# Optimization experiments

Hardware: AMD Instinct MI355X
Metric: run time of the kernel (lower is better)

## Reference

```python
import jax, jax.numpy as jnp
import numpy as np

D_MODEL = 1024
HEADS = 16
DILATION = 4
LN_EPS = 1e-5


def setup_inputs() -> dict:
    key = jax.random.key(0)
    ks = jax.random.split(key, 11)
    B, S, D = 2, 4096, D_MODEL
    x = jax.random.normal(ks[0], (B, S, D), dtype=jnp.float32)
    def lin(k):
        kw, kb = jax.random.split(k)
        W = jax.random.normal(kw, (D, D), dtype=jnp.float32) * 0.02  # torch Linear layout [out, in]
        b = jax.random.normal(kb, (D,), dtype=jnp.float32) * 0.02
        return W, b
    Wq, bq = lin(ks[1])
    Wk, bk = lin(ks[2])
    Wv, bv = lin(ks[3])
    Wf, bf = lin(ks[4])
    gamma = jnp.ones((D,), dtype=jnp.float32)
    beta = jnp.zeros((D,), dtype=jnp.float32)
    return {"x": x, "Wq": Wq, "bq": bq, "Wk": Wk, "bk": bk,
            "Wv": Wv, "bv": bv, "Wf": Wf, "bf": bf,
            "gamma": gamma, "beta": beta}


def _layer_norm(x, gamma, beta):
    mu = jnp.mean(x, axis=-1, keepdims=True)
    var = jnp.mean(jnp.square(x - mu), axis=-1, keepdims=True)
    return (x - mu) * jax.lax.rsqrt(var + LN_EPS) * gamma + beta


def reference(x, Wq, bq, Wk, bk, Wv, bv, Wf, bf, gamma, beta):
    B, S, D = x.shape
    dil, H = DILATION, HEADS
    dh = D // H
    pad = (-S) % dil  # padding_size
    xp = jnp.pad(x, ((0, 0), (0, pad), (0, 0)))
    Sp = S + pad
    L = Sp // dil
    # strided (atrous) regrouping: [B, Sp, D] -> [B*dil, L, D]
    xr = xp.reshape(B, L, dil, D).transpose(0, 2, 1, 3).reshape(B * dil, L, D)
    q = xr @ Wq.T + bq
    k = xr @ Wk.T + bk
    v = xr @ Wv.T + bv
    # split heads: [B*dil, H, L, dh]
    q = q.reshape(B * dil, L, H, dh).transpose(0, 2, 1, 3)
    k = k.reshape(B * dil, L, H, dh).transpose(0, 2, 1, 3)
    v = v.reshape(B * dil, L, H, dh).transpose(0, 2, 1, 3)
    scores = jnp.einsum('bhqd,bhkd->bhqk', q, k) / jnp.sqrt(jnp.float32(dh))
    probs = jax.nn.softmax(scores, axis=-1)
    ctx = jnp.einsum('bhqk,bhkd->bhqd', probs, v)
    # merge heads and undo atrous regrouping
    ctx = ctx.transpose(0, 2, 1, 3).reshape(B * dil, L, D)
    ctx = ctx.reshape(B, dil, L, D).transpose(0, 2, 1, 3).reshape(B, Sp, D)
    ctx = ctx[:, :S]
    atted = ctx @ Wf.T + bf  # dropout p=0.0
    final = _layer_norm(atted + x, gamma, beta)
    return (final, atted)
```

## Files before the change

### kernel.cpp

```cpp
#include <hip/hip_runtime.h>
#include <hip/hip_bf16.h>
#include <cstdint>
#include <cstddef>

constexpr int B_  = 2;
constexpr int S_  = 4096;
constexpr int D_  = 1024;
constexpr int H_  = 16;
constexpr int DH_ = 64;
constexpr int DIL = 4;
constexpr int L_  = S_ / DIL;
constexpr int M_  = B_ * S_;

typedef __attribute__((ext_vector_type(8))) short short8;
typedef __attribute__((ext_vector_type(4))) float f32x4;

__device__ __forceinline__ unsigned short f2b(float f) {
    union { float f; unsigned u; } v;
    v.f = f;
    unsigned r = v.u + 0x7fff + ((v.u >> 16) & 1);
    return (unsigned short)(r >> 16);
}

__device__ __forceinline__ unsigned pkbf(float a, float b) {
    float2 t; t.x = a; t.y = b;
    __hip_bfloat162 h = __float22bfloat162_rn(t);
    union { __hip_bfloat162 h; unsigned u; } c; c.h = h;
    return c.u;
}

__device__ __forceinline__ int xcd_swz(int orig, int nwg) {
    int q = nwg >> 3, r = nwg & 7;
    int xcd = orig & 7, idx = orig >> 3;
    return (xcd < r ? xcd * (q + 1) : r * (q + 1) + (xcd - r) * q) + idx;
}

#define GLOAD16(gptr, lptr)                                                    \
    __builtin_amdgcn_global_load_lds(                                          \
        (const __attribute__((address_space(1))) void*)(gptr),                 \
        (__attribute__((address_space(3))) void*)(lptr), 16, 0, 0)

__global__ __launch_bounds__(256)
void conv_f2b(const float* __restrict__ in, unsigned short* __restrict__ out, int n4) {
    int i = blockIdx.x * 256 + threadIdx.x;
    if (i < n4) {
        float4 v = reinterpret_cast<const float4*>(in)[i];
        ushort4 o;
        o.x = f2b(v.x); o.y = f2b(v.y); o.z = f2b(v.z); o.w = f2b(v.w);
        reinterpret_cast<ushort4*>(out)[i] = o;
    }
}

__global__ __launch_bounds__(256)
void conv_w4(const float* __restrict__ w0, const float* __restrict__ w1,
             const float* __restrict__ w2, const float* __restrict__ w3,
             unsigned short* __restrict__ out) {
    int bid = blockIdx.x;
    int which = bid >> 10;
    const float* src = (which == 0) ? w0 : (which == 1) ? w1 : (which == 2) ? w2 : w3;
    int i = (bid & 1023) * 256 + threadIdx.x;
    float4 v = reinterpret_cast<const float4*>(src)[i];
    ushort4 o;
    o.x = f2b(v.x); o.y = f2b(v.y); o.z = f2b(v.z); o.w = f2b(v.w);
    reinterpret_cast<ushort4*>(out + (size_t)which * D_ * D_)[i] = o;
}

template <int OUT_BF16>
__global__ __launch_bounds__(256)
void gemm_mfma(const unsigned short* __restrict__ A,
               const unsigned short* __restrict__ W,
               const float* __restrict__ bias,
               void* __restrict__ Cout, int M, int N, int K) {
    __shared__ unsigned short As[2][128 * 64];
    __shared__ unsigned short Bs[2][128 * 64];

    const int tid  = threadIdx.x;
    const int lane = tid & 63, wave = tid >> 6;
    const int l15 = lane & 15, l4 = lane >> 4;
    const int wr = wave >> 1, wc = wave & 1;
    const int gx = N >> 7;
    const int wg = xcd_swz(blockIdx.x, gridDim.x);
    const int bm = (wg / gx) * 128, bn = (wg % gx) * 128;

    auto stage = [&](int k0, int buf) {
        #pragma unroll
        for (int i = 0; i < 4; ++i) {
            int ch = i * 256 + wave * 64 + lane;
            int r = ch >> 3, c8 = ch & 7;
            const unsigned short* ga = A + (size_t)(bm + r) * K + k0 + c8 * 8;
            GLOAD16(ga, (char*)&As[buf][0] + (size_t)(i * 256 + wave * 64) * 16);
            const unsigned short* gb = W + (size_t)(bn + r) * K + k0 + c8 * 8;
            GLOAD16(gb, (char*)&Bs[buf][0] + (size_t)(i * 256 + wave * 64) * 16);
        }
    };

    f32x4 acc[4][4] = {};

    stage(0, 0);
    __syncthreads();
    int cur = 0;

    for (int k0 = 0; k0 < K; k0 += 64) {
        if (k0 + 64 < K) stage(k0 + 64, cur ^ 1);

        #pragma unroll
        for (int ks = 0; ks < 2; ++ks) {
            short8 af[4], bf[4];
            #pragma unroll
            for (int mi = 0; mi < 4; ++mi)
                af[mi] = *reinterpret_cast<const short8*>(
                    &As[cur][(wr * 64 + mi * 16 + l15) * 64 + ks * 32 + l4 * 8]);
            #pragma unroll
            for (int ni = 0; ni < 4; ++ni)
                bf[ni] = *reinterpret_cast<const short8*>(
                    &Bs[cur][(wc * 64 + ni * 16 + l15) * 64 + ks * 32 + l4 * 8]);
            #pragma unroll
            for (int mi = 0; mi < 4; ++mi)
                #pragma unroll
                for (int ni = 0; ni < 4; ++ni)
                    acc[mi][ni] = __builtin_amdgcn_mfma_f32_16x16x32_bf16(
                        af[mi], bf[ni], acc[mi][ni], 0, 0, 0);
        }
        __syncthreads();
        cur ^= 1;
    }

    #pragma unroll
    for (int ni = 0; ni < 4; ++ni) {
        int col = bn + wc * 64 + ni * 16 + l15;
        float bv = bias[col];
        #pragma unroll
        for (int mi = 0; mi < 4; ++mi) {
            #pragma unroll
            for (int r = 0; r < 4; ++r) {
                int row = bm + wr * 64 + mi * 16 + l4 * 4 + r;
                float v = acc[mi][ni][r] + bv;
                if (OUT_BF16)
                    ((unsigned short*)Cout)[(size_t)row * N + col] = f2b(v);
                else
                    ((float*)Cout)[(size_t)row * N + col] = v;
            }
        }
    }
}

__global__ __launch_bounds__(256)
void gemm_qkv(const unsigned short* __restrict__ A,
              const unsigned short* __restrict__ W,
              const float* __restrict__ bq, const float* __restrict__ bk,
              const float* __restrict__ bv,
              unsigned short* __restrict__ Qb, unsigned short* __restrict__ Kb,
              unsigned short* __restrict__ Vb, int M, int K) {
    __shared__ unsigned short As[2][128 * 64];
    __shared__ unsigned short Bs[2][128 * 64];

    const int tid  = threadIdx.x;
    const int lane = tid & 63, wave = tid >> 6;
    const int l15 = lane & 15, l4 = lane >> 4;
    const int wr = wave >> 1, wc = wave & 1;
    const int gx = 24;
    const int wg = xcd_swz(blockIdx.x, gridDim.x);
    const int bm = (wg / gx) * 128, bn = (wg % gx) * 128;

    auto stage = [&](int k0, int buf) {
        #pragma unroll
        for (int i = 0; i < 4; ++i) {
            int ch = i * 256 + wave * 64 + lane;
            int r = ch >> 3, c8 = ch & 7;
            const unsigned short* ga = A + (size_t)(bm + r) * K + k0 + c8 * 8;
            GLOAD16(ga, (char*)&As[buf][0] + (size_t)(i * 256 + wave * 64) * 16);
            const unsigned short* gb = W + (size_t)(bn + r) * K + k0 + c8 * 8;
            GLOAD16(gb, (char*)&Bs[buf][0] + (size_t)(i * 256 + wave * 64) * 16);
        }
    };

    f32x4 acc[4][4] = {};

    stage(0, 0);
    __syncthreads();
    int cur = 0;

    for (int k0 = 0; k0 < K; k0 += 64) {
        if (k0 + 64 < K) stage(k0 + 64, cur ^ 1);

        #pragma unroll
        for (int ks = 0; ks < 2; ++ks) {
            short8 af[4], bf[4];
            #pragma unroll
            for (int mi = 0; mi < 4; ++mi)
                af[mi] = *reinterpret_cast<const short8*>(
                    &As[cur][(wr * 64 + mi * 16 + l15) * 64 + ks * 32 + l4 * 8]);
            #pragma unroll
            for (int ni = 0; ni < 4; ++ni)
                bf[ni] = *reinterpret_cast<const short8*>(
                    &Bs[cur][(wc * 64 + ni * 16 + l15) * 64 + ks * 32 + l4 * 8]);
            #pragma unroll
            for (int mi = 0; mi < 4; ++mi)
                #pragma unroll
                for (int ni = 0; ni < 4; ++ni)
                    acc[mi][ni] = __builtin_amdgcn_mfma_f32_16x16x32_bf16(
                        af[mi], bf[ni], acc[mi][ni], 0, 0, 0);
        }
        __syncthreads();
        cur ^= 1;
    }

    const int seg = bn >> 10;
    const float* bp = (seg == 0) ? bq : (seg == 1) ? bk : bv;
    unsigned short* ob = (seg == 0) ? Qb : (seg == 1) ? Kb : Vb;
    const float qs = (seg == 0) ? 0.125f : 1.0f;
    const int cb = bn & 1023;

    #pragma unroll
    for (int ni = 0; ni < 4; ++ni) {
        int col = cb + wc * 64 + ni * 16 + l15;
        float bvv = bp[col];
        #pragma unroll
        for (int mi = 0; mi < 4; ++mi) {
            #pragma unroll
            for (int r = 0; r < 4; ++r) {
                int row = bm + wr * 64 + mi * 16 + l4 * 4 + r;
                ob[(size_t)row * 1024 + col] = f2b((acc[mi][ni][r] + bvv) * qs);
            }
        }
    }
}

__global__ __launch_bounds__(256)
void tvt(const unsigned short* __restrict__ Vb, unsigned short* __restrict__ Vtg) {
    __shared__ unsigned short Ts[64 * 64];
    const int tid = threadIdx.x;
    const int blk = blockIdx.x;
    const int lt = blk & 15;
    const int h  = (blk >> 4) & 15;
    const int bd = blk >> 8;
    const int b = bd >> 2, dd = bd & 3;
    const size_t rowbase = (size_t)b * S_;

    #pragma unroll
    for (int i = 0; i < 2; ++i) {
        int ch = i * 256 + tid;
        int lloc = ch >> 3, c8 = ch & 7;
        short8 v = *reinterpret_cast<const short8*>(
            Vb + (rowbase + (size_t)(lt * 64 + lloc) * DIL + dd) * D_ + h * 64 + c8 * 8);
        #pragma unroll
        for (int j = 0; j < 8; ++j) {
            int dh = c8 * 8 + j;
            Ts[dh * 64 + (((lloc >> 3) ^ (dh & 7)) * 8) + (lloc & 7)] = (unsigned short)v[j];
        }
    }
    __syncthreads();

    const size_t obase = ((size_t)(bd * 16 + h) * 64) * L_;
    #pragma unroll
    for (int i = 0; i < 2; ++i) {
        int ch = i * 256 + tid;
        int dh = ch >> 3, c = ch & 7;
        uint4 val = *reinterpret_cast<const uint4*>(&Ts[dh * 64 + ((c ^ (dh & 7)) * 8)]);
        *reinterpret_cast<uint4*>(Vtg + obase + (size_t)dh * L_ + lt * 64 + c * 8) = val;
    }
}

__global__ __launch_bounds__(256)
void attn_mfma(const unsigned short* __restrict__ Q,
               const unsigned short* __restrict__ K,
               const unsigned short* __restrict__ Vtg,
               unsigned short* __restrict__ O) {
    __shared__ unsigned short Ks[2][64 * 64];
    __shared__ unsigned short Vs[2][64 * 64];
    __shared__ unsigned short Ps[4][1024];

    const int tid = threadIdx.x;
    const int lane = tid & 63, wave = tid >> 6;
    const int l15 = lane & 15, l4 = lane >> 4;
    const int blk = xcd_swz(blockIdx.x, gridDim.x);
    const int qt = blk & 15;
    const int h  = (blk >> 4) & 15;
    const int bd = blk >> 8;
    const int b = bd >> 2, dd = bd & 3;
    const size_t rowbase = (size_t)b * S_;
    const int colbase = h * DH_;

    short8 qf[2];
    {
        int q = qt * 64 + wave * 16 + l15;
        const unsigned short* qp =
            Q + (rowbase + (size_t)q * DIL + dd) * D_ + colbase;
        qf[0] = *reinterpret_cast<const short8*>(qp + l4 * 8);
        qf[1] = *reinterpret_cast<const short8*>(qp + 32 + l4 * 8);
    }

    const unsigned short* vbase = Vtg + ((size_t)(bd * 16 + h) * 64) * L_;

    auto stageK = [&](int kt, int buf) {
        #pragma unroll
        for (int i = 0; i < 2; ++i) {
            int key = i * 32 + wave * 8 + (lane >> 3);
            int srcc = (lane & 7) ^ (lane >> 3);
            const unsigned short* g =
                K + (rowbase + (size_t)(kt * 64 + key) * DIL + dd) * D_ + colbase + srcc * 8;
            GLOAD16(g, (char*)&Ks[buf][0] + (size_t)(i * 256 + wave * 64) * 16);
        }
    };
    auto stageV = [&](int kt, int buf) {
        #pragma unroll
        for (int i = 0; i < 2; ++i) {
            int dh = i * 32 + wave * 8 + (lane >> 3);
            int srcc = (lane & 7) ^ (lane >> 3);
            const unsigned short* g = vbase + (size_t)dh * L_ + kt * 64 + srcc * 8;
            GLOAD16(g, (char*)&Vs[buf][0] + (size_t)(i * 256 + wave * 64) * 16);
        }
    };

    f32x4 oT[4] = {};
    float m_run = -1e30f, l_run = 0.f;

    stageK(0, 0);
    stageV(0, 0);
    __syncthreads();

    constexpr int NT = L_ / 64;
    for (int kt = 0; kt < NT; ++kt) {
        int cur = kt & 1, nxt = cur ^ 1;
        if (kt < NT - 1) {
            stageK(kt + 1, nxt);
            stageV(kt + 1, nxt);
        }

        f32x4 sT[4];
        #pragma unroll
        for (int n = 0; n < 4; ++n) {
            int row = n * 16 + l15;
            short8 kf0 = *reinterpret_cast<const short8*>(
                &Ks[cur][row * 64 + ((0 * 4 + l4) ^ (l15 & 7)) * 8]);
            short8 kf1 = *reinterpret_cast<const short8*>(
                &Ks[cur][row * 64 + ((1 * 4 + l4) ^ (l15 & 7)) * 8]);
            f32x4 z = {0.f, 0.f, 0.f, 0.f};
            z = __builtin_amdgcn_mfma_f32_16x16x32_bf16(kf0, qf[0], z, 0, 0, 0);
            z = __builtin_amdgcn_mfma_f32_16x16x32_bf16(kf1, qf[1], z, 0, 0, 0);
            sT[n] = z;
        }

        float mx = -1e30f;
        #pragma unroll
        for (int n = 0; n < 4; ++n)
            #pragma unroll
            for (int r = 0; r < 4; ++r) mx = fmaxf(mx, sT[n][r]);
        mx = fmaxf(mx, __shfl_xor(mx, 16));
        mx = fmaxf(mx, __shfl_xor(mx, 32));
        float m_new = fmaxf(m_run, mx);
        float scale = __expf(m_run - m_new);
        float p[4][4], rsum = 0.f;
        #pragma unroll
        for (int n = 0; n < 4; ++n)
            #pragma unroll
            for (int r = 0; r < 4; ++r) {
                p[n][r] = __expf(sT[n][r] - m_new);
                rsum += p[n][r];
            }
        rsum += __shfl_xor(rsum, 16);
        rsum += __shfl_xor(rsum, 32);
        l_run = l_run * scale + rsum;
        m_run = m_new;
        #pragma unroll
        for (int nd = 0; nd < 4; ++nd) oT[nd] *= scale;

        #pragma unroll
        for (int n = 0; n < 4; ++n) {
            uint2 w;
            w.x = pkbf(p[n][0], p[n][1]);
            w.y = pkbf(p[n][2], p[n][3]);
            int c = n * 2 + (l4 >> 1);
            int pc = c ^ (l15 & 7);
            *reinterpret_cast<uint2*>(&Ps[wave][l15 * 64 + pc * 8 + (l4 & 1) * 4]) = w;
        }
        short8 pb0 = *reinterpret_cast<const short8*>(
            &Ps[wave][l15 * 64 + ((0 * 4 + l4) ^ (l15 & 7)) * 8]);
        short8 pb1 = *reinterpret_cast<const short8*>(
            &Ps[wave][l15 * 64 + ((1 * 4 + l4) ^ (l15 & 7)) * 8]);

        #pragma unroll
        for (int ks = 0; ks < 2; ++ks) {
            short8 pb = ks ? pb1 : pb0;
            #pragma unroll
            for (int nd = 0; nd < 4; ++nd) {
                short8 vf = *reinterpret_cast<const short8*>(
                    &Vs[cur][(nd * 16 + l15) * 64 + ((ks * 4 + l4) ^ (l15 & 7)) * 8]);
                oT[nd] = __builtin_amdgcn_mfma_f32_16x16x32_bf16(vf, pb, oT[nd], 0, 0, 0);
            }
        }

        __syncthreads();
    }

    unsigned short* Es = &Ps[0][0];
    float inv = 1.f / l_run;
    #pragma unroll
    for (int nd = 0; nd < 4; ++nd) {
        uint2 w;
        w.x = pkbf(oT[nd][0] * inv, oT[nd][1] * inv);
        w.y = pkbf(oT[nd][2] * inv, oT[nd][3] * inv);
        int chunk = nd * 2 + (l4 >> 1);
        int pc = chunk ^ (l15 & 7);
        *reinterpret_cast<uint2*>(&Es[wave * 1024 + l15 * 64 + pc * 8 + (l4 & 1) * 4]) = w;
    }
    __syncthreads();
    {
        int row = lane >> 2;
        int q = qt * 64 + wave * 16 + row;
        unsigned short* op = O + (rowbase + (size_t)q * DIL + dd) * D_ + colbase;
        #pragma unroll
        for (int i = 0; i < 2; ++i) {
            int c = (lane & 3) * 2 + i;
            int pc = c ^ (row & 7);
            uint4 val = *reinterpret_cast<const uint4*>(&Es[wave * 1024 + row * 64 + pc * 8]);
            *reinterpret_cast<uint4*>(op + c * 8) = val;
        }
    }
}

__global__ __launch_bounds__(256)
void add_ln(const float* __restrict__ atted, const float* __restrict__ x,
            const float* __restrict__ gamma, const float* __restrict__ beta,
            float* __restrict__ out) {
    __shared__ float red[8];
    const int tid = threadIdx.x;
    const size_t base = (size_t)blockIdx.x * D_;

    float4 a  = *reinterpret_cast<const float4*>(atted + base + tid * 4);
    float4 xv = *reinterpret_cast<const float4*>(x + base + tid * 4);
    float v0 = a.x + xv.x, v1 = a.y + xv.y, v2 = a.z + xv.z, v3 = a.w + xv.w;

    float s = v0 + v1 + v2 + v3;
    #pragma unroll
    for (int o = 1; o < 64; o <<= 1) s += __shfl_xor(s, o);
    if ((tid & 63) == 0) red[tid >> 6] = s;
    __syncthreads();
    float mean = (red[0] + red[1] + red[2] + red[3]) * (1.0f / D_);

    float d0 = v0 - mean, d1 = v1 - mean, d2 = v2 - mean, d3 = v3 - mean;
    float sq = d0 * d0 + d1 * d1 + d2 * d2 + d3 * d3;
    #pragma unroll
    for (int o = 1; o < 64; o <<= 1) sq += __shfl_xor(sq, o);
    if ((tid & 63) == 0) red[4 + (tid >> 6)] = sq;
    __syncthreads();
    float var = (red[4] + red[5] + red[6] + red[7]) * (1.0f / D_);
    float inv = rsqrtf(var + 1e-5f);

    float4 g  = *reinterpret_cast<const float4*>(gamma + tid * 4);
    float4 bb = *reinterpret_cast<const float4*>(beta + tid * 4);
    float4 o4;
    o4.x = d0 * inv * g.x + bb.x;
    o4.y = d1 * inv * g.y + bb.y;
    o4.z = d2 * inv * g.z + bb.z;
    o4.w = d3 * inv * g.w + bb.w;
    *reinterpret_cast<float4*>(out + base + tid * 4) = o4;
}

extern "C" void kernel_launch(void* const* d_in, const int* in_sizes, int n_in,
                              void* d_out, int out_size, void* d_ws, size_t ws_size,
                              hipStream_t stream) {
    const float* x     = (const float*)d_in[0];
    const float* Wq    = (const float*)d_in[1];
    const float* bq    = (const float*)d_in[2];
    const float* Wk    = (const float*)d_in[3];
    const float* bk    = (const float*)d_in[4];
    const float* Wv    = (const float*)d_in[5];
    const float* bv    = (const float*)d_in[6];
    const float* Wf    = (const float*)d_in[7];
    const float* bf    = (const float*)d_in[8];
    const float* gamma = (const float*)d_in[9];
    const float* beta  = (const float*)d_in[10];

    float* final_out = (float*)d_out;
    float* atted     = final_out + (size_t)M_ * D_;

    unsigned short* xb  = (unsigned short*)d_ws;
    unsigned short* Wqb = xb  + (size_t)M_ * D_;
    unsigned short* Wkb = Wqb + (size_t)D_ * D_;
    unsigned short* Wvb = Wkb + (size_t)D_ * D_;
    unsigned short* Wfb = Wvb + (size_t)D_ * D_;
    unsigned short* Qb  = Wfb + (size_t)D_ * D_;
    unsigned short* Kb  = Qb  + (size_t)M_ * D_;
    unsigned short* Vb  = Kb  + (size_t)M_ * D_;
    unsigned short* Vtg = Vb  + (size_t)M_ * D_;
    unsigned short* ctxb = xb;

    conv_f2b<<<dim3(M_ * D_ / 4 / 256), 256, 0, stream>>>(x, xb, M_ * D_ / 4);
    conv_w4<<<dim3(4096), 256, 0, stream>>>(Wq, Wk, Wv, Wf, Wqb);

    gemm_qkv<<<dim3((3072 / 128) * (M_ / 128)), 256, 0, stream>>>(
        xb, Wqb, bq, bk, bv, Qb, Kb, Vb, M_, D_);

    tvt<<<dim3(DIL * B_ * H_ * (L_ / 64)), 256, 0, stream>>>(Vb, Vtg);

    attn_mfma<<<dim3(DIL * B_ * H_ * (L_ / 64)), 256, 0, stream>>>(Qb, Kb, Vtg, ctxb);

    gemm_mfma<0><<<dim3((D_ / 128) * (M_ / 128)), 256, 0, stream>>>(
        ctxb, Wfb, bf, atted, M_, D_, D_);

    add_ln<<<dim3(M_), 256, 0, stream>>>(atted, x, gamma, beta, final_out);
}
```

Baseline: 319.7 us.

## Use partial vmcnt waits with raw barriers to keep prefetch in flight

In both GEMM kernels and the attention kernel, the full __syncthreads after issuing the next tile's async global-to-LDS loads is replaced by a partial s_waitcnt vmcnt that waits only for the current tile's loads, followed by a raw s_barrier. The goal is to let the next tile's prefetch stay in flight while the current tile is computed, instead of draining every outstanding load at each barrier. The attention kernel also raises wave priority around its MFMA blocks with s_setprio. The risk is correctness: the vmcnt counts must match the number of outstanding loads per thread, and a raw barrier does not flush pending LDS or memory operations the way __syncthreads does.

```diff
diff --git a/kernel.cpp b/kernel.cpp
--- a/kernel.cpp
+++ b/kernel.cpp
@@ -39,6 +39,8 @@
     __builtin_amdgcn_global_load_lds(                                          \
         (const __attribute__((address_space(1))) void*)(gptr),                 \
         (__attribute__((address_space(3))) void*)(lptr), 16, 0, 0)
+
+#define VMCNT(N) asm volatile("s_waitcnt vmcnt(" #N ")" ::: "memory")
 
 __global__ __launch_bounds__(256)
 void conv_f2b(const float* __restrict__ in, unsigned short* __restrict__ out, int n4) {
@@ -97,11 +99,16 @@
     f32x4 acc[4][4] = {};
 
     stage(0, 0);
-    __syncthreads();
     int cur = 0;
 
     for (int k0 = 0; k0 < K; k0 += 64) {
-        if (k0 + 64 < K) stage(k0 + 64, cur ^ 1);
+        if (k0 + 64 < K) {
+            stage(k0 + 64, cur ^ 1);
+            VMCNT(8);
+        } else {
+            VMCNT(0);
+        }
+        __builtin_amdgcn_s_barrier();
 
         #pragma unroll
         for (int ks = 0; ks < 2; ++ks) {
@@ -121,7 +128,7 @@
                     acc[mi][ni] = __builtin_amdgcn_mfma_f32_16x16x32_bf16(
                         af[mi], bf[ni], acc[mi][ni], 0, 0, 0);
         }
-        __syncthreads();
+        __builtin_amdgcn_s_barrier();
         cur ^= 1;
     }
 
@@ -177,11 +184,16 @@
     f32x4 acc[4][4] = {};
 
     stage(0, 0);
-    __syncthreads();
     int cur = 0;
 
     for (int k0 = 0; k0 < K; k0 += 64) {
-        if (k0 + 64 < K) stage(k0 + 64, cur ^ 1);
+        if (k0 + 64 < K) {
+            stage(k0 + 64, cur ^ 1);
+            VMCNT(8);
+        } else {
+            VMCNT(0);
+        }
+        __builtin_amdgcn_s_barrier();
 
         #pragma unroll
         for (int ks = 0; ks < 2; ++ks) {
@@ -201,7 +213,7 @@
                     acc[mi][ni] = __builtin_amdgcn_mfma_f32_16x16x32_bf16(
                         af[mi], bf[ni], acc[mi][ni], 0, 0, 0);
         }
-        __syncthreads();
+        __builtin_amdgcn_s_barrier();
         cur ^= 1;
     }
 
@@ -317,7 +329,6 @@
 
     stageK(0, 0);
     stageV(0, 0);
-    __syncthreads();
 
     constexpr int NT = L_ / 64;
     for (int kt = 0; kt < NT; ++kt) {
@@ -325,9 +336,14 @@
         if (kt < NT - 1) {
             stageK(kt + 1, nxt);
             stageV(kt + 1, nxt);
-        }
+            VMCNT(4);
+        } else {
+            VMCNT(0);
+        }
+        __builtin_amdgcn_s_barrier();
 
         f32x4 sT[4];
+        __builtin_amdgcn_s_setprio(1);
         #pragma unroll
         for (int n = 0; n < 4; ++n) {
             int row = n * 16 + l15;
@@ -340,6 +356,7 @@
             z = __builtin_amdgcn_mfma_f32_16x16x32_bf16(kf1, qf[1], z, 0, 0, 0);
             sT[n] = z;
         }
+        __builtin_amdgcn_s_setprio(0);
 
         float mx = -1e30f;
         #pragma unroll
@@ -379,6 +396,7 @@
         short8 pb1 = *reinterpret_cast<const short8*>(
             &Ps[wave][l15 * 64 + ((1 * 4 + l4) ^ (l15 & 7)) * 8]);
 
+        __builtin_amdgcn_s_setprio(1);
         #pragma unroll
         for (int ks = 0; ks < 2; ++ks) {
             short8 pb = ks ? pb1 : pb0;
@@ -389,8 +407,9 @@
                 oT[nd] = __builtin_amdgcn_mfma_f32_16x16x32_bf16(vf, pb, oT[nd], 0, 0, 0);
             }
         }
-
-        __syncthreads();
+        __builtin_amdgcn_s_setprio(0);
+
+        __builtin_amdgcn_s_barrier();
     }
 
     unsigned short* Es = &Ps[0][0];
```

Measured after the change: 304.1 us. 1.05x faster.
